# Performance work log

Measured on AMD Instinct MI355X. Metric: run time of the kernel, lower is better.

## Reference

```python
import jax, jax.numpy as jnp
import numpy as np

N = 21  # nodes per graph (20 laser sectors + 1 robot node)
MAX_RANGE = 10.0
_bound = np.linspace(-np.pi / 2 - 0.03, np.pi / 2, 21, dtype=np.float32)[:-1]
_angles = _bound + np.float32(np.pi / 20)
ANGLE_FEAT = jnp.asarray(np.stack([np.sin(_angles), np.cos(_angles)], 1), dtype=jnp.float32)  # [20,2]


def _build_nodes(state24):
    # state24: [B,24] -> node features [B,21,7]
    B = state24.shape[0]
    laser = state24[:, :20, None] / MAX_RANGE                       # [B,20,1]
    angle = jnp.broadcast_to(ANGLE_FEAT[None], (B, 20, 2))          # [B,20,2]
    sector = jnp.concatenate([laser, angle, jnp.zeros((B, 20, 4), state24.dtype)], -1)  # [B,20,7]
    robot = jnp.concatenate([jnp.zeros((B, 1, 3), state24.dtype), state24[:, None, 20:]], -1)  # [B,1,7]
    return jnp.concatenate([sector, robot], axis=1)                 # [B,21,7]


def _gatv2(x, Wl, Wr, att, bias, heads, dim):
    # GATv2 over a fully-connected graph with self-loops (dense all-pairs).
    # e_ij = att . leaky_relu(Wl x_j + Wr x_i); alpha = softmax_j; out_i = sum_j alpha_ij (Wl x_j)
    B = x.shape[0]
    gl = (x @ Wl).reshape(B, N, heads, dim)  # source transform [B,j,H,D]
    gr = (x @ Wr).reshape(B, N, heads, dim)  # target transform [B,i,H,D]
    s = jax.nn.leaky_relu(gl[:, None] + gr[:, :, None], negative_slope=0.2)  # [B,i,j,H,D]
    e = jnp.einsum('bijhd,hd->bijh', s, att)                                  # [B,i,j,H]
    alpha = jax.nn.softmax(e, axis=2)                                          # softmax over sources j
    out = jnp.einsum('bijh,bjhd->bihd', alpha, gl).reshape(B, N, heads * dim)
    return out + bias


def setup_inputs() -> dict:
    key = jax.random.key(0)
    ks = jax.random.split(key, 16)
    r = lambda k, shape, s: (jax.random.normal(k, shape, dtype=jnp.float32) * s)
    B = 1024
    return {
        'state24': jax.random.normal(ks[0], (B, 24), dtype=jnp.float32),
        'Wl1': r(ks[1], (7, 256), 0.3), 'Wr1': r(ks[2], (7, 256), 0.3),
        'att1': r(ks[3], (4, 64), 0.1), 'b1': r(ks[4], (256,), 0.02),
        'Wl2': r(ks[5], (256, 64), 0.06), 'Wr2': r(ks[6], (256, 64), 0.06),
        'att2': r(ks[7], (1, 64), 0.1), 'b2': r(ks[8], (64,), 0.02),
        'fc1_w': r(ks[9], (64, 256), 0.12), 'fc1_b': r(ks[10], (256,), 0.02),
        'fc2_w': r(ks[11], (256, 256), 0.06), 'fc2_b': r(ks[12], (256,), 0.02),
        'fc3_w': r(ks[13], (256, 2), 0.06), 'fc3_b': r(ks[14], (2,), 0.02),
    }


def reference(state24, Wl1, Wr1, att1, b1, Wl2, Wr2, att2, b2,
              fc1_w, fc1_b, fc2_w, fc2_b, fc3_w, fc3_b):
    x = _build_nodes(state24)                               # [B,21,7]
    h = jax.nn.elu(_gatv2(x, Wl1, Wr1, att1, b1, 4, 64))    # [B,21,256]
    h = _gatv2(h, Wl2, Wr2, att2, b2, 1, 64)                # [B,21,64]
    nfv = jnp.mean(h, axis=1)                               # global_mean_pool -> [B,64]
    h = jax.nn.relu(nfv @ fc1_w + fc1_b)
    h = jax.nn.relu(h @ fc2_w + fc2_b)
    return jnp.tanh(h @ fc3_w + fc3_b)                      # [B,2]
```

## Files before the change

### kernel.cpp

```cpp
#include <hip/hip_runtime.h>
#include <hip/hip_fp16.h>
#include <math.h>

#define PI_D 3.141592653589793

typedef _Float16 h2 __attribute__((ext_vector_type(2)));
typedef _Float16 h8 __attribute__((ext_vector_type(8)));
typedef unsigned short us8 __attribute__((ext_vector_type(8)));
typedef __fp16 f16v2 __attribute__((ext_vector_type(2)));
typedef __fp16 f16v8 __attribute__((ext_vector_type(8)));
typedef float f32x4 __attribute__((ext_vector_type(4)));

#define STR1 264
#define STR2 66
#define EPS 24

static __device__ __forceinline__ h2 pack_h2(float a, float b) {
    return __builtin_bit_cast(h2, __builtin_amdgcn_cvt_pkrtz(a, b));
}

static __device__ __forceinline__ float fdot2(h2 a, h2 b, float c) {
    return __builtin_amdgcn_fdot2(__builtin_bit_cast(f16v2, a),
                                  __builtin_bit_cast(f16v2, b), c, false);
}

static __device__ __forceinline__ h8 habs8(h8 x) {
    us8 u = __builtin_bit_cast(us8, x);
    us8 m = {0x7fff, 0x7fff, 0x7fff, 0x7fff, 0x7fff, 0x7fff, 0x7fff, 0x7fff};
    return __builtin_bit_cast(h8, (us8)(u & m));
}

static __device__ __forceinline__ f32x4 mfma16(h8 a, h8 b, f32x4 c) {
    return __builtin_amdgcn_mfma_f32_16x16x32_f16(
        __builtin_bit_cast(f16v8, a), __builtin_bit_cast(f16v8, b), c, 0, 0, 0);
}

__global__ __launch_bounds__(256) void pack_weights_kernel(
    const float* __restrict__ Wl2, const float* __restrict__ Wr2,
    const float* __restrict__ fc1_w, const float* __restrict__ fc2_w,
    h8* __restrict__ ws)
{
    int idx = blockIdx.x * 256 + threadIdx.x;
    if (idx < 4096) {
        const float* W = idx < 2048 ? Wl2 : Wr2;
        int t = idx & 2047;
        int ntile = t >> 9, rem = t & 511;
        int kchunk = rem >> 6, lane = rem & 63;
        int n = ntile * 16 + (lane & 15);
        int k0 = kchunk * 32 + (lane >> 4) * 8;
        h8 o;
        #pragma unroll
        for (int j = 0; j < 8; ++j) o[j] = (_Float16)W[(k0 + j) * 64 + n];
        ws[idx] = o;
    } else if (idx < 6144) {
        int t = idx - 4096;
        int k2 = t >> 6, c = t & 63;
        h8 o;
        #pragma unroll
        for (int q = 0; q < 4; ++q) {
            o[2 * q]     = (_Float16)fc1_w[(2 * k2) * 256 + 4 * c + q];
            o[2 * q + 1] = (_Float16)fc1_w[(2 * k2 + 1) * 256 + 4 * c + q];
        }
        ws[idx] = o;
    } else {
        int t = idx - 6144;
        int k2 = t >> 6, c = t & 63;
        h8 o;
        #pragma unroll
        for (int q = 0; q < 4; ++q) {
            o[2 * q]     = (_Float16)fc2_w[(2 * k2) * 256 + 4 * c + q];
            o[2 * q + 1] = (_Float16)fc2_w[(2 * k2 + 1) * 256 + 4 * c + q];
        }
        ws[idx] = o;
    }
}

__global__ __launch_bounds__(256, 4) void actor_fused_kernel(
    const float* __restrict__ state24,
    const float* __restrict__ Wl1, const float* __restrict__ Wr1,
    const float* __restrict__ att1, const float* __restrict__ b1,
    const float* __restrict__ att2, const float* __restrict__ b2,
    const float* __restrict__ fc1_b, const float* __restrict__ fc2_b,
    const float* __restrict__ fc3_w, const float* __restrict__ fc3_b,
    const h8* __restrict__ wsL, const h8* __restrict__ wsR,
    const h8* __restrict__ wsF1, const h8* __restrict__ wsF2,
    float* __restrict__ out, int B)
{
    const int bix = blockIdx.x;
    if (bix >= B) return;
    const int tid = threadIdx.x;

    __shared__ float sinL[20], cosL[20], laserL[20], robotL[4];
    __shared__ __align__(16) h2 attLh[128];
    __shared__ __align__(16) float att2L[64];
    __shared__ __align__(16) _Float16 gr1h[32 * STR1];
    __shared__ __align__(16) union {
        struct { _Float16 gl1h[21 * STR1];
                 float eP[84 * EPS];
                 float uv[168]; } p1;
        struct { float gl2[24 * STR2]; float gr2[24 * STR2]; float e2[504];
                 float red[4][256];
                 _Float16 nfvh[64]; _Float16 hah[256]; _Float16 hbh[256]; } p2;
    } U;

    if (tid < 20) {
        double step = (PI_D + 0.03) / 20.0;
        float bound = (float)(-PI_D / 2.0 - 0.03 + (double)tid * step);
        float ang = bound + (float)(PI_D / 20.0);
        sinL[tid] = sinf(ang);
        cosL[tid] = cosf(ang);
        laserL[tid] = state24[bix * 24 + tid] * 0.1f;
    }
    if (tid >= 32 && tid < 36) robotL[tid - 32] = state24[bix * 24 + 20 + (tid - 32)];
    if (tid < 128) {
        float2 ap = ((const float2*)att1)[tid];
        attLh[tid] = pack_h2(ap.x, ap.y);
    }
    if (tid < 64) att2L[tid] = att2[tid];
    __syncthreads();

    {
        float wl[7], wr[7];
        #pragma unroll
        for (int k = 0; k < 7; k++) { wl[k] = Wl1[k * 256 + tid]; wr[k] = Wr1[k * 256 + tid]; }
        #pragma unroll
        for (int n = 0; n < 20; n++) {
            float l = laserL[n], s = sinL[n], c = cosL[n];
            U.p1.gl1h[n * STR1 + tid] = (_Float16)(l * wl[0] + s * wl[1] + c * wl[2]);
            gr1h[n * STR1 + tid]     = (_Float16)(l * wr[0] + s * wr[1] + c * wr[2]);
        }
        float r0 = robotL[0], r1 = robotL[1], r2 = robotL[2], r3 = robotL[3];
        U.p1.gl1h[20 * STR1 + tid] = (_Float16)(r0 * wl[3] + r1 * wl[4] + r2 * wl[5] + r3 * wl[6]);
        gr1h[20 * STR1 + tid]     = (_Float16)(r0 * wr[3] + r1 * wr[4] + r2 * wr[5] + r3 * wr[6]);
    }
    __syncthreads();

    if (tid < 168) {
        int r = tid < 84 ? tid : tid - 84;
        int h = r / 21, idx = r - h * 21;
        const _Float16* rowp = (tid < 84 ? U.p1.gl1h : gr1h) + idx * STR1 + h * 64;
        const h8* row8 = (const h8*)rowp;
        const h2* ar = attLh + h * 32;
        float l0 = 0.f, l1 = 0.f;
        #pragma unroll
        for (int ch = 0; ch < 8; ++ch) {
            h8 g = row8[ch];
            l0 = fdot2(__builtin_shufflevector(g, g, 0, 1), ar[ch * 4 + 0], l0);
            l1 = fdot2(__builtin_shufflevector(g, g, 2, 3), ar[ch * 4 + 1], l1);
            l0 = fdot2(__builtin_shufflevector(g, g, 4, 5), ar[ch * 4 + 2], l0);
            l1 = fdot2(__builtin_shufflevector(g, g, 6, 7), ar[ch * 4 + 3], l1);
        }
        U.p1.uv[tid] = l0 + l1;
    }
    __syncthreads();

    {
        const int h = tid >> 6;
        const int lane = tid & 63;
        h2 ar[32];
        #pragma unroll
        for (int q = 0; q < 32; ++q) ar[q] = attLh[h * 32 + q];
        const float* uvU = U.p1.uv + h * 21;
        const float* uvV = U.p1.uv + 84 + h * 21;

        for (int it = 0; it < 7; ++it) {
            int q = it * 64 + lane;
            if (q < 441) {
                int i = q / 21;
                int j = q - i * 21;
                const h8* gA8 = (const h8*)(U.p1.gl1h + j * STR1 + h * 64);
                const h8* gB8 = (const h8*)(gr1h + i * STR1 + h * 64);
                float m0 = 0.f, m1 = 0.f;
                #pragma unroll
                for (int ch = 0; ch < 8; ++ch) {
                    h8 x = gA8[ch] + gB8[ch];
                    h8 ax = habs8(x);
                    m0 = fdot2(__builtin_shufflevector(ax, ax, 0, 1), ar[ch * 4 + 0], m0);
                    m1 = fdot2(__builtin_shufflevector(ax, ax, 2, 3), ar[ch * 4 + 1], m1);
                    m0 = fdot2(__builtin_shufflevector(ax, ax, 4, 5), ar[ch * 4 + 2], m0);
                    m1 = fdot2(__builtin_shufflevector(ax, ax, 6, 7), ar[ch * 4 + 3], m1);
                }
                U.p1.eP[(h * 21 + i) * EPS + j] = 0.6f * (uvU[j] + uvV[i]) + 0.4f * (m0 + m1);
            }
        }
    }
    __syncthreads();

    if (tid < 84) {
        float* row = U.p1.eP + tid * EPS;
        float m = row[0];
        #pragma unroll
        for (int j = 1; j < 21; j++) m = fmaxf(m, row[j]);
        float s = 0.f;
        #pragma unroll
        for (int j = 0; j < 21; j++) { float v = __expf(row[j] - m); row[j] = v; s += v; }
        float r = 1.f / s;
        #pragma unroll
        for (int j = 0; j < 21; j++) row[j] *= r;
    }
    __syncthreads();

    {
        h8* z8 = (h8*)gr1h;
        h8 zz = {(_Float16)0.f, (_Float16)0.f, (_Float16)0.f, (_Float16)0.f,
                 (_Float16)0.f, (_Float16)0.f, (_Float16)0.f, (_Float16)0.f};
        for (int z = tid; z < 363; z += 256) z8[693 + z] = zz;

        const int h = tid >> 6, c = tid & 63;
        const int col = h * 64 + c;
        float glv[21];
        #pragma unroll
        for (int j = 0; j < 21; ++j) glv[j] = (float)U.p1.gl1h[j * STR1 + col];
        float bb = b1[col];
        for (int i = 0; i < 21; ++i) {
            const float4* ar4 = (const float4*)(U.p1.eP + (h * 21 + i) * EPS);
            float4 q0 = ar4[0], q1 = ar4[1], q2 = ar4[2], q3 = ar4[3], q4 = ar4[4];
            float a20 = U.p1.eP[(h * 21 + i) * EPS + 20];
            float acc;
            acc = q0.x * glv[0];
            acc = fmaf(q0.y, glv[1], acc);
            acc = fmaf(q0.z, glv[2], acc);
            acc = fmaf(q0.w, glv[3], acc);
            acc = fmaf(q1.x, glv[4], acc);
            acc = fmaf(q1.y, glv[5], acc);
            acc = fmaf(q1.z, glv[6], acc);
            acc = fmaf(q1.w, glv[7], acc);
            acc = fmaf(q2.x, glv[8], acc);
            acc = fmaf(q2.y, glv[9], acc);
            acc = fmaf(q2.z, glv[10], acc);
            acc = fmaf(q2.w, glv[11], acc);
            acc = fmaf(q3.x, glv[12], acc);
            acc = fmaf(q3.y, glv[13], acc);
            acc = fmaf(q3.z, glv[14], acc);
            acc = fmaf(q3.w, glv[15], acc);
            acc = fmaf(q4.x, glv[16], acc);
            acc = fmaf(q4.y, glv[17], acc);
            acc = fmaf(q4.z, glv[18], acc);
            acc = fmaf(q4.w, glv[19], acc);
            acc = fmaf(a20, glv[20], acc);
            float v = acc + bb;
            v = v > 0.f ? v : __expf(v) - 1.f;
            gr1h[i * STR1 + col] = (_Float16)v;
        }
    }
    __syncthreads();

    {
        const int lane = tid & 63;
        const int w = tid >> 6;
        const int mrow = lane & 15;
        const int quad = lane >> 4;
        const h8* hA0 = (const h8*)(gr1h + mrow * STR1 + quad * 8);
        const h8* hA1 = (const h8*)(gr1h + (16 + mrow) * STR1 + quad * 8);
        const h8* bL = wsL + w * 512 + lane;
        const h8* bR = wsR + w * 512 + lane;
        f32x4 aL0 = {0.f, 0.f, 0.f, 0.f}, aL1 = {0.f, 0.f, 0.f, 0.f};
        f32x4 aR0 = {0.f, 0.f, 0.f, 0.f}, aR1 = {0.f, 0.f, 0.f, 0.f};
        #pragma unroll
        for (int kc = 0; kc < 8; ++kc) {
            h8 A0 = hA0[kc * 4];
            h8 A1 = hA1[kc * 4];
            h8 BL = bL[kc * 64];
            h8 BR = bR[kc * 64];
            aL0 = mfma16(A0, BL, aL0);
            aL1 = mfma16(A1, BL, aL1);
            aR0 = mfma16(A0, BR, aR0);
            aR1 = mfma16(A1, BR, aR1);
        }
        const int col = w * 16 + mrow;
        #pragma unroll
        for (int r = 0; r < 4; ++r) {
            int row0 = quad * 4 + r;
            U.p2.gl2[row0 * STR2 + col] = aL0[r];
            U.p2.gr2[row0 * STR2 + col] = aR0[r];
            int row1 = 16 + row0;
            if (row1 < 24) {
                U.p2.gl2[row1 * STR2 + col] = aL1[r];
                U.p2.gr2[row1 * STR2 + col] = aR1[r];
            }
        }
    }
    __syncthreads();

    for (int it = 0; it < 2; ++it) {
        int t = it * 256 + tid;
        if (t < 441) {
            int i = t / 21;
            int j = t - i * 21;
            const float2* gA = (const float2*)(U.p2.gl2 + j * STR2);
            const float2* gB = (const float2*)(U.p2.gr2 + i * STR2);
            const float2* aa = (const float2*)att2L;
            float l0 = 0.f, l1 = 0.f, m0 = 0.f, m1 = 0.f;
            #pragma unroll
            for (int dp = 0; dp < 32; ++dp) {
                float2 va = gA[dp], vb = gB[dp], a = aa[dp];
                float x0 = va.x + vb.x, x1 = va.y + vb.y;
                l0 = fmaf(a.x, x0, l0); m0 = fmaf(a.x, fabsf(x0), m0);
                l1 = fmaf(a.y, x1, l1); m1 = fmaf(a.y, fabsf(x1), m1);
            }
            U.p2.e2[t] = 0.6f * (l0 + l1) + 0.4f * (m0 + m1);
        }
    }
    __syncthreads();

    if (tid < 24) {
        float* row = U.p2.e2 + tid * 21;
        if (tid < 21) {
            float m = row[0];
            #pragma unroll
            for (int j = 1; j < 21; j++) m = fmaxf(m, row[j]);
            float s = 0.f;
            #pragma unroll
            for (int j = 0; j < 21; j++) { float v = __expf(row[j] - m); row[j] = v; s += v; }
            float r = 1.f / s;
            #pragma unroll
            for (int j = 0; j < 21; j++) row[j] *= r;
        } else {
            #pragma unroll
            for (int j = 0; j < 21; j++) row[j] = 0.f;
        }
    }
    __syncthreads();

    {
        int d = tid & 63, g = tid >> 6;
        float sacc = 0.f;
        #pragma unroll
        for (int m = 0; m < 6; ++m) {
            int i = g + 4 * m;
            const float* al = U.p2.e2 + i * 21;
            float acc = 0.f;
            #pragma unroll
            for (int j = 0; j < 21; ++j) acc = fmaf(al[j], U.p2.gl2[j * STR2 + d], acc);
            sacc += acc;
        }
        U.p2.red[g][d] = sacc;
    }
    __syncthreads();
    if (tid < 64) {
        float v = (U.p2.red[0][tid] + U.p2.red[1][tid] + U.p2.red[2][tid] + U.p2.red[3][tid])
                  * (1.f / 21.f) + b2[tid];
        U.p2.nfvh[tid] = (_Float16)v;
    }
    __syncthreads();

    {
        int c = tid & 63, g = tid >> 6;
        const h2* x2p = (const h2*)U.p2.nfvh;
        float4 acc = {0.f, 0.f, 0.f, 0.f};
        #pragma unroll
        for (int kk = 0; kk < 8; ++kk) {
            int k2 = g * 8 + kk;
            h8 w = wsF1[k2 * 64 + c];
            h2 x2 = x2p[k2];
            acc.x = fdot2(__builtin_shufflevector(w, w, 0, 1), x2, acc.x);
            acc.y = fdot2(__builtin_shufflevector(w, w, 2, 3), x2, acc.y);
            acc.z = fdot2(__builtin_shufflevector(w, w, 4, 5), x2, acc.z);
            acc.w = fdot2(__builtin_shufflevector(w, w, 6, 7), x2, acc.w);
        }
        ((float4*)U.p2.red[g])[c] = acc;
    }
    __syncthreads();
    {
        float v = U.p2.red[0][tid] + U.p2.red[1][tid] + U.p2.red[2][tid] + U.p2.red[3][tid]
                  + fc1_b[tid];
        U.p2.hah[tid] = (_Float16)fmaxf(v, 0.f);
    }
    __syncthreads();

    {
        int c = tid & 63, g = tid >> 6;
        const h8* haH = (const h8*)U.p2.hah;
        float4 acc = {0.f, 0.f, 0.f, 0.f};
#define FC2_STEP(q, p)                                                          \
        {                                                                       \
            int k2 = g * 32 + (q) * 4 + (p);                                    \
            h8 w = wsF2[k2 * 64 + c];                                           \
            h2 x2 = __builtin_shufflevector(xa, xa, 2 * (p), 2 * (p) + 1);      \
            acc.x = fdot2(__builtin_shufflevector(w, w, 0, 1), x2, acc.x);      \
            acc.y = fdot2(__builtin_shufflevector(w, w, 2, 3), x2, acc.y);      \
            acc.z = fdot2(__builtin_shufflevector(w, w, 4, 5), x2, acc.z);      \
            acc.w = fdot2(__builtin_shufflevector(w, w, 6, 7), x2, acc.w);      \
        }
        #pragma unroll
        for (int q = 0; q < 8; ++q) {
            h8 xa = haH[g * 8 + q];
            FC2_STEP(q, 0)
            FC2_STEP(q, 1)
            FC2_STEP(q, 2)
            FC2_STEP(q, 3)
        }
#undef FC2_STEP
        ((float4*)U.p2.red[g])[c] = acc;
    }
    __syncthreads();
    {
        float v = U.p2.red[0][tid] + U.p2.red[1][tid] + U.p2.red[2][tid] + U.p2.red[3][tid]
                  + fc2_b[tid];
        U.p2.hbh[tid] = (_Float16)fmaxf(v, 0.f);
    }
    __syncthreads();

    if (tid < 128) {
        int o = tid >> 6, l = tid & 63;
        float s = 0.f;
        #pragma unroll
        for (int m = 0; m < 4; m++) {
            int k = l + 64 * m;
            s = fmaf((float)U.p2.hbh[k], fc3_w[k * 2 + o], s);
        }
        #pragma unroll
        for (int off = 32; off >= 1; off >>= 1) s += __shfl_down(s, off, 64);
        if (l == 0) out[bix * 2 + o] = tanhf(s + fc3_b[o]);
    }
}

extern "C" void kernel_launch(void* const* d_in, const int* in_sizes, int n_in,
                              void* d_out, int out_size, void* d_ws, size_t ws_size,
                              hipStream_t stream) {
    const float* state24 = (const float*)d_in[0];
    const float* Wl1 = (const float*)d_in[1];
    const float* Wr1 = (const float*)d_in[2];
    const float* att1 = (const float*)d_in[3];
    const float* b1 = (const float*)d_in[4];
    const float* Wl2 = (const float*)d_in[5];
    const float* Wr2 = (const float*)d_in[6];
    const float* att2 = (const float*)d_in[7];
    const float* b2 = (const float*)d_in[8];
    const float* fc1_w = (const float*)d_in[9];
    const float* fc1_b = (const float*)d_in[10];
    const float* fc2_w = (const float*)d_in[11];
    const float* fc2_b = (const float*)d_in[12];
    const float* fc3_w = (const float*)d_in[13];
    const float* fc3_b = (const float*)d_in[14];
    float* out = (float*)d_out;

    h8* ws = (h8*)d_ws;
    const h8* wsL = ws;
    const h8* wsR = ws + 2048;
    const h8* wsF1 = ws + 4096;
    const h8* wsF2 = ws + 6144;

    pack_weights_kernel<<<56, 256, 0, stream>>>(Wl2, Wr2, fc1_w, fc2_w, ws);

    int B = in_sizes[0] / 24;
    actor_fused_kernel<<<B, 256, 0, stream>>>(
        state24, Wl1, Wr1, att1, b1, att2, b2,
        fc1_b, fc2_b, fc3_w, fc3_b,
        wsL, wsR, wsF1, wsF2, out, B);
}
```

Before: 117.6 us.

## Use fp16 packed dot products for layer-2 attention and shrink shared buffers

Layer-2 attention scores now run on fp16 copies of gl2/gr2 using packed fdot2 with the abs trick, the same path layer 1 uses, instead of fp32 scalar loops. The linear term is split into per-node u/v dot products added inside the softmax. The 0.4 factor is folded into the packed attention weights, and the layer-1 scores likewise defer the linear term to the softmax. Layer-1 node features are computed two columns per thread with packed stores, gr1h shrinks to 22 rows with less zero-padding, and the layer-2 aggregation caches gl2 in registers and reads weights as float4. The cost is lower precision in the layer-2 scores and more shared memory for the extra fp16 copies.

```diff
diff --git a/kernel.cpp b/kernel.cpp
--- a/kernel.cpp
+++ b/kernel.cpp
@@ -13,7 +13,9 @@
 
 #define STR1 264
 #define STR2 66
+#define STR2H 72
 #define EPS 24
+#define EPS2 24
 
 static __device__ __forceinline__ h2 pack_h2(float a, float b) {
     return __builtin_bit_cast(h2, __builtin_amdgcn_cvt_pkrtz(a, b));
@@ -92,13 +94,17 @@
 
     __shared__ float sinL[20], cosL[20], laserL[20], robotL[4];
     __shared__ __align__(16) h2 attLh[128];
-    __shared__ __align__(16) float att2L[64];
-    __shared__ __align__(16) _Float16 gr1h[32 * STR1];
+    __shared__ __align__(16) h2 att2Lh[32];
+    __shared__ __align__(16) _Float16 gr1h[22 * STR1];
     __shared__ __align__(16) union {
         struct { _Float16 gl1h[21 * STR1];
                  float eP[84 * EPS];
                  float uv[168]; } p1;
-        struct { float gl2[24 * STR2]; float gr2[24 * STR2]; float e2[504];
+        struct { float gl2[24 * STR2];
+                 _Float16 gl2h[24 * STR2H];
+                 _Float16 gr2h[24 * STR2H];
+                 float e2[24 * EPS2];
+                 float u2v2[42];
                  float red[4][256];
                  _Float16 nfvh[64]; _Float16 hah[256]; _Float16 hbh[256]; } p2;
     } U;
@@ -114,24 +120,46 @@
     if (tid >= 32 && tid < 36) robotL[tid - 32] = state24[bix * 24 + 20 + (tid - 32)];
     if (tid < 128) {
         float2 ap = ((const float2*)att1)[tid];
-        attLh[tid] = pack_h2(ap.x, ap.y);
-    }
-    if (tid < 64) att2L[tid] = att2[tid];
-    __syncthreads();
-
-    {
-        float wl[7], wr[7];
-        #pragma unroll
-        for (int k = 0; k < 7; k++) { wl[k] = Wl1[k * 256 + tid]; wr[k] = Wr1[k * 256 + tid]; }
-        #pragma unroll
-        for (int n = 0; n < 20; n++) {
-            float l = laserL[n], s = sinL[n], c = cosL[n];
-            U.p1.gl1h[n * STR1 + tid] = (_Float16)(l * wl[0] + s * wl[1] + c * wl[2]);
-            gr1h[n * STR1 + tid]     = (_Float16)(l * wr[0] + s * wr[1] + c * wr[2]);
-        }
-        float r0 = robotL[0], r1 = robotL[1], r2 = robotL[2], r3 = robotL[3];
-        U.p1.gl1h[20 * STR1 + tid] = (_Float16)(r0 * wl[3] + r1 * wl[4] + r2 * wl[5] + r3 * wl[6]);
-        gr1h[20 * STR1 + tid]     = (_Float16)(r0 * wr[3] + r1 * wr[4] + r2 * wr[5] + r3 * wr[6]);
+        attLh[tid] = pack_h2(0.4f * ap.x, 0.4f * ap.y);
+    }
+    if (tid >= 128 && tid < 160) {
+        float2 ap = ((const float2*)att2)[tid - 128];
+        att2Lh[tid - 128] = pack_h2(0.4f * ap.x, 0.4f * ap.y);
+    }
+    __syncthreads();
+
+    {
+        const int d2 = tid & 127;
+        const int half = tid >> 7;
+        float2 wl[7], wr[7];
+        #pragma unroll
+        for (int k = 0; k < 7; k++) {
+            wl[k] = ((const float2*)Wl1)[k * 128 + d2];
+            wr[k] = ((const float2*)Wr1)[k * 128 + d2];
+        }
+        const int base = half * 11;
+        #pragma unroll
+        for (int nn = 0; nn < 11; ++nn) {
+            int node = base + nn;
+            if (node < 21) {
+                float a0, a1, b0, b1v;
+                if (node < 20) {
+                    float l = laserL[node], s = sinL[node], c = cosL[node];
+                    a0 = l * wl[0].x + s * wl[1].x + c * wl[2].x;
+                    a1 = l * wl[0].y + s * wl[1].y + c * wl[2].y;
+                    b0 = l * wr[0].x + s * wr[1].x + c * wr[2].x;
+                    b1v = l * wr[0].y + s * wr[1].y + c * wr[2].y;
+                } else {
+                    float r0 = robotL[0], r1 = robotL[1], r2 = robotL[2], r3 = robotL[3];
+                    a0 = r0 * wl[3].x + r1 * wl[4].x + r2 * wl[5].x + r3 * wl[6].x;
+                    a1 = r0 * wl[3].y + r1 * wl[4].y + r2 * wl[5].y + r3 * wl[6].y;
+                    b0 = r0 * wr[3].x + r1 * wr[4].x + r2 * wr[5].x + r3 * wr[6].x;
+                    b1v = r0 * wr[3].y + r1 * wr[4].y + r2 * wr[5].y + r3 * wr[6].y;
+                }
+                ((h2*)(U.p1.gl1h + node * STR1))[d2] = pack_h2(a0, a1);
+                ((h2*)(gr1h + node * STR1))[d2] = pack_h2(b0, b1v);
+            }
+        }
     }
     __syncthreads();
 
@@ -160,8 +188,6 @@
         h2 ar[32];
         #pragma unroll
         for (int q = 0; q < 32; ++q) ar[q] = attLh[h * 32 + q];
-        const float* uvU = U.p1.uv + h * 21;
-        const float* uvV = U.p1.uv + 84 + h * 21;
 
         for (int it = 0; it < 7; ++it) {
             int q = it * 64 + lane;
@@ -180,32 +206,40 @@
                     m0 = fdot2(__builtin_shufflevector(ax, ax, 4, 5), ar[ch * 4 + 2], m0);
                     m1 = fdot2(__builtin_shufflevector(ax, ax, 6, 7), ar[ch * 4 + 3], m1);
                 }
-                U.p1.eP[(h * 21 + i) * EPS + j] = 0.6f * (uvU[j] + uvV[i]) + 0.4f * (m0 + m1);
+                U.p1.eP[(h * 21 + i) * EPS + j] = m0 + m1;
             }
         }
     }
     __syncthreads();
 
     if (tid < 84) {
+        int h = tid / 21, i = tid - h * 21;
         float* row = U.p1.eP + tid * EPS;
-        float m = row[0];
-        #pragma unroll
-        for (int j = 1; j < 21; j++) m = fmaxf(m, row[j]);
+        const float* uu = U.p1.uv + h * 21;
+        float vi = 1.5f * U.p1.uv[84 + h * 21 + i];
+        float ebuf[21];
+        float m = -1e30f;
+        #pragma unroll
+        for (int j = 0; j < 21; j++) {
+            float e = row[j] + 1.5f * uu[j] + vi;
+            ebuf[j] = e;
+            m = fmaxf(m, e);
+        }
         float s = 0.f;
         #pragma unroll
-        for (int j = 0; j < 21; j++) { float v = __expf(row[j] - m); row[j] = v; s += v; }
+        for (int j = 0; j < 21; j++) { float v = __expf(ebuf[j] - m); ebuf[j] = v; s += v; }
         float r = 1.f / s;
         #pragma unroll
-        for (int j = 0; j < 21; j++) row[j] *= r;
-    }
-    __syncthreads();
-
-    {
-        h8* z8 = (h8*)gr1h;
-        h8 zz = {(_Float16)0.f, (_Float16)0.f, (_Float16)0.f, (_Float16)0.f,
-                 (_Float16)0.f, (_Float16)0.f, (_Float16)0.f, (_Float16)0.f};
-        for (int z = tid; z < 363; z += 256) z8[693 + z] = zz;
-
+        for (int j = 0; j < 21; j++) row[j] = ebuf[j] * r;
+    }
+    __syncthreads();
+
+    {
+        if (tid < 33) {
+            h8 zz = {(_Float16)0.f, (_Float16)0.f, (_Float16)0.f, (_Float16)0.f,
+                     (_Float16)0.f, (_Float16)0.f, (_Float16)0.f, (_Float16)0.f};
+            ((h8*)gr1h)[21 * 33 + tid] = zz;
+        }
         const int h = tid >> 6, c = tid & 63;
         const int col = h * 64 + c;
         float glv[21];
@@ -250,8 +284,9 @@
         const int w = tid >> 6;
         const int mrow = lane & 15;
         const int quad = lane >> 4;
+        int rowA1 = 16 + mrow; if (rowA1 > 21) rowA1 = 21;
         const h8* hA0 = (const h8*)(gr1h + mrow * STR1 + quad * 8);
-        const h8* hA1 = (const h8*)(gr1h + (16 + mrow) * STR1 + quad * 8);
+        const h8* hA1 = (const h8*)(gr1h + rowA1 * STR1 + quad * 8);
         const h8* bL = wsL + w * 512 + lane;
         const h8* bR = wsR + w * 512 + lane;
         f32x4 aL0 = {0.f, 0.f, 0.f, 0.f}, aL1 = {0.f, 0.f, 0.f, 0.f};
@@ -272,49 +307,81 @@
         for (int r = 0; r < 4; ++r) {
             int row0 = quad * 4 + r;
             U.p2.gl2[row0 * STR2 + col] = aL0[r];
-            U.p2.gr2[row0 * STR2 + col] = aR0[r];
+            U.p2.gl2h[row0 * STR2H + col] = (_Float16)aL0[r];
+            U.p2.gr2h[row0 * STR2H + col] = (_Float16)aR0[r];
             int row1 = 16 + row0;
-            if (row1 < 24) {
+            if (row1 < 21) {
                 U.p2.gl2[row1 * STR2 + col] = aL1[r];
-                U.p2.gr2[row1 * STR2 + col] = aR1[r];
+                U.p2.gl2h[row1 * STR2H + col] = (_Float16)aL1[r];
+                U.p2.gr2h[row1 * STR2H + col] = (_Float16)aR1[r];
             }
         }
     }
     __syncthreads();
 
-    for (int it = 0; it < 2; ++it) {
-        int t = it * 256 + tid;
-        if (t < 441) {
-            int i = t / 21;
-            int j = t - i * 21;
-            const float2* gA = (const float2*)(U.p2.gl2 + j * STR2);
-            const float2* gB = (const float2*)(U.p2.gr2 + i * STR2);
-            const float2* aa = (const float2*)att2L;
-            float l0 = 0.f, l1 = 0.f, m0 = 0.f, m1 = 0.f;
+    {
+        h2 ar2[32];
+        #pragma unroll
+        for (int q = 0; q < 32; ++q) ar2[q] = att2Lh[q];
+
+        #pragma unroll
+        for (int it = 0; it < 2; ++it) {
+            int t = it * 256 + tid;
+            if (t < 441) {
+                int i = t / 21;
+                int j = t - i * 21;
+                const h8* gA8 = (const h8*)(U.p2.gl2h + j * STR2H);
+                const h8* gB8 = (const h8*)(U.p2.gr2h + i * STR2H);
+                float m0 = 0.f, m1 = 0.f;
+                #pragma unroll
+                for (int ch = 0; ch < 8; ++ch) {
+                    h8 x = gA8[ch] + gB8[ch];
+                    h8 ax = habs8(x);
+                    m0 = fdot2(__builtin_shufflevector(ax, ax, 0, 1), ar2[ch * 4 + 0], m0);
+                    m1 = fdot2(__builtin_shufflevector(ax, ax, 2, 3), ar2[ch * 4 + 1], m1);
+                    m0 = fdot2(__builtin_shufflevector(ax, ax, 4, 5), ar2[ch * 4 + 2], m0);
+                    m1 = fdot2(__builtin_shufflevector(ax, ax, 6, 7), ar2[ch * 4 + 3], m1);
+                }
+                U.p2.e2[i * EPS2 + j] = m0 + m1;
+            } else if (t < 483) {
+                int u = t - 441;
+                int r = u < 21 ? u : u - 21;
+                const _Float16* rowp = (u < 21 ? U.p2.gl2h : U.p2.gr2h) + r * STR2H;
+                const h8* row8 = (const h8*)rowp;
+                float l0 = 0.f, l1 = 0.f;
+                #pragma unroll
+                for (int ch = 0; ch < 8; ++ch) {
+                    h8 g = row8[ch];
+                    l0 = fdot2(__builtin_shufflevector(g, g, 0, 1), ar2[ch * 4 + 0], l0);
+                    l1 = fdot2(__builtin_shufflevector(g, g, 2, 3), ar2[ch * 4 + 1], l1);
+                    l0 = fdot2(__builtin_shufflevector(g, g, 4, 5), ar2[ch * 4 + 2], l0);
+                    l1 = fdot2(__builtin_shufflevector(g, g, 6, 7), ar2[ch * 4 + 3], l1);
+                }
+                U.p2.u2v2[u] = l0 + l1;
+            }
+        }
+    }
+    __syncthreads();
+
+    if (tid < 24) {
+        float* row = U.p2.e2 + tid * EPS2;
+        if (tid < 21) {
+            const float* uu = U.p2.u2v2;
+            float vi = 1.5f * U.p2.u2v2[21 + tid];
+            float ebuf[21];
+            float m = -1e30f;
             #pragma unroll
-            for (int dp = 0; dp < 32; ++dp) {
-                float2 va = gA[dp], vb = gB[dp], a = aa[dp];
-                float x0 = va.x + vb.x, x1 = va.y + vb.y;
-                l0 = fmaf(a.x, x0, l0); m0 = fmaf(a.x, fabsf(x0), m0);
-                l1 = fmaf(a.y, x1, l1); m1 = fmaf(a.y, fabsf(x1), m1);
+            for (int j = 0; j < 21; j++) {
+                float e = row[j] + 1.5f * uu[j] + vi;
+                ebuf[j] = e;
+                m = fmaxf(m, e);
             }
-            U.p2.e2[t] = 0.6f * (l0 + l1) + 0.4f * (m0 + m1);
-        }
-    }
-    __syncthreads();
-
-    if (tid < 24) {
-        float* row = U.p2.e2 + tid * 21;
-        if (tid < 21) {
-            float m = row[0];
-            #pragma unroll
-            for (int j = 1; j < 21; j++) m = fmaxf(m, row[j]);
             float s = 0.f;
             #pragma unroll
-            for (int j = 0; j < 21; j++) { float v = __expf(row[j] - m); row[j] = v; s += v; }
+            for (int j = 0; j < 21; j++) { float v = __expf(ebuf[j] - m); ebuf[j] = v; s += v; }
             float r = 1.f / s;
             #pragma unroll
-            for (int j = 0; j < 21; j++) row[j] *= r;
+            for (int j = 0; j < 21; j++) row[j] = ebuf[j] * r;
         } else {
             #pragma unroll
             for (int j = 0; j < 21; j++) row[j] = 0.f;
@@ -324,14 +391,38 @@
 
     {
         int d = tid & 63, g = tid >> 6;
+        float glv2[21];
+        #pragma unroll
+        for (int j = 0; j < 21; ++j) glv2[j] = U.p2.gl2[j * STR2 + d];
         float sacc = 0.f;
         #pragma unroll
         for (int m = 0; m < 6; ++m) {
             int i = g + 4 * m;
-            const float* al = U.p2.e2 + i * 21;
-            float acc = 0.f;
-            #pragma unroll
-            for (int j = 0; j < 21; ++j) acc = fmaf(al[j], U.p2.gl2[j * STR2 + d], acc);
+            const float4* ar4 = (const float4*)(U.p2.e2 + i * EPS2);
+            float4 q0 = ar4[0], q1 = ar4[1], q2 = ar4[2], q3 = ar4[3], q4 = ar4[4];
+            float a20 = U.p2.e2[i * EPS2 + 20];
+            float acc;
+            acc = q0.x * glv2[0];
+            acc = fmaf(q0.y, glv2[1], acc);
+            acc = fmaf(q0.z, glv2[2], acc);
+            acc = fmaf(q0.w, glv2[3], acc);
+            acc = fmaf(q1.x, glv2[4], acc);
+            acc = fmaf(q1.y, glv2[5], acc);
+            acc = fmaf(q1.z, glv2[6], acc);
+            acc = fmaf(q1.w, glv2[7], acc);
+            acc = fmaf(q2.x, glv2[8], acc);
+            acc = fmaf(q2.y, glv2[9], acc);
+            acc = fmaf(q2.z, glv2[10], acc);
+            acc = fmaf(q2.w, glv2[11], acc);
+            acc = fmaf(q3.x, glv2[12], acc);
+            acc = fmaf(q3.y, glv2[13], acc);
+            acc = fmaf(q3.z, glv2[14], acc);
+            acc = fmaf(q3.w, glv2[15], acc);
+            acc = fmaf(q4.x, glv2[16], acc);
+            acc = fmaf(q4.y, glv2[17], acc);
+            acc = fmaf(q4.z, glv2[18], acc);
+            acc = fmaf(q4.w, glv2[19], acc);
+            acc = fmaf(a20, glv2[20], acc);
             sacc += acc;
         }
         U.p2.red[g][d] = sacc;
```

Measured after the change: 115.3 us. Within noise of the previous version (-1.9%).
